# Performance work log

Measured on AMD Instinct MI355X. Metric: run time of the kernel, lower is better.

The kernel has to match this reference:

```python
import jax, jax.numpy as jnp
import numpy as np
import math

B, S, D, H, DFF = 4, 2048, 1024, 16, 4096
DK = D // 2  # 512; per-head dim = DK // H = 32
LN_EPS = 1e-3  # keras LayerNormalization default


def gelu_tanh(x):
    c = math.sqrt(2.0 / math.pi)
    return 0.5 * x * (1.0 + jnp.tanh(c * (x + 0.044715 * x * x * x)))


def layer_norm(z, g, b):
    mu = jnp.mean(z, axis=-1, keepdims=True)
    var = jnp.mean(jnp.square(z - mu), axis=-1, keepdims=True)
    return (z - mu) * jax.lax.rsqrt(var + LN_EPS) * g + b


def setup_inputs() -> dict:
    key = jax.random.key(0)
    ks = jax.random.split(key, 10)
    s = 0.02
    return {
        "x": jax.random.normal(ks[0], (B, S, D), dtype=jnp.float32),
        "mask": jnp.zeros((1, 1, S, S), dtype=jnp.float32),
        "Wq": jax.random.normal(ks[1], (D, DK), dtype=jnp.float32) * s,
        "bq": jnp.zeros((DK,), jnp.float32),
        "Wk": jax.random.normal(ks[2], (D, DK), dtype=jnp.float32) * s,
        "bk": jnp.zeros((DK,), jnp.float32),
        "Wv": jax.random.normal(ks[3], (D, DK), dtype=jnp.float32) * s,
        "bv": jnp.zeros((DK,), jnp.float32),
        "Wo": jax.random.normal(ks[4], (DK, D), dtype=jnp.float32) * s,
        "bo": jnp.zeros((D,), jnp.float32),
        "W1": jax.random.normal(ks[5], (D, DFF), dtype=jnp.float32) * s,
        "b1": jnp.zeros((DFF,), jnp.float32),
        "W2": jax.random.normal(ks[6], (DFF, D), dtype=jnp.float32) * s,
        "b2": jnp.zeros((D,), jnp.float32),
        "g1": jnp.ones((D,), jnp.float32),
        "be1": jnp.zeros((D,), jnp.float32),
        "g2": jnp.ones((D,), jnp.float32),
        "be2": jnp.zeros((D,), jnp.float32),
    }


def reference(x, mask, Wq, bq, Wk, bk, Wv, bv, Wo, bo, W1, b1, W2, b2, g1, be1, g2, be2):
    dh = DK // H
    # QKV projections: D -> DK total, split over H heads
    q = (x @ Wq + bq).reshape(B, S, H, dh).transpose(0, 2, 1, 3)  # [B,H,S,dh]
    k = (x @ Wk + bk).reshape(B, S, H, dh).transpose(0, 2, 1, 3)
    v = (x @ Wv + bv).reshape(B, S, H, dh).transpose(0, 2, 1, 3)
    # NOTE: source scales by sqrt(d_k)=sqrt(DK), not per-head dim
    scores = jnp.einsum("bhqd,bhkd->bhqk", q, k) / jnp.sqrt(jnp.asarray(DK, x.dtype))
    scores = scores + (-1e9) * mask
    w = jax.nn.softmax(scores, axis=-1)
    o = jnp.einsum("bhqk,bhkd->bhqd", w, v)  # [B,H,S,dh]
    o = o.transpose(0, 2, 1, 3).reshape(B, S, DK)
    attn_out = o @ Wo + bo  # [B,S,D]
    h1 = layer_norm(x + attn_out, g1, be1)
    # NOTE: source applies GELU AFTER the second Dense
    ff = gelu_tanh((h1 @ W1 + b1) @ W2 + b2)
    return layer_norm(h1 + ff, g2, be2)
```

## Files before the change

### kernel.cpp

```cpp
#include <hip/hip_runtime.h>

typedef unsigned short u16;
typedef unsigned int   u32;
typedef short s16x8 __attribute__((ext_vector_type(8)));
typedef float f32x4 __attribute__((ext_vector_type(4)));
typedef u32   u32x2 __attribute__((ext_vector_type(2)));
typedef s16x8 __attribute__((may_alias)) s16x8_a;
typedef f32x4 __attribute__((may_alias)) f32x4_a;
typedef u32x2 __attribute__((may_alias)) u32x2_a;

#define S_LEN   2048
#define D_MODEL 1024
#define DK_DIM  512
#define DFF_DIM 4096
#define MS_ROWS 8192

__device__ __forceinline__ u16 f2bf(float f) {
  union { float f; unsigned u; } x; x.f = f;
  unsigned r = x.u + 0x7fffu + ((x.u >> 16) & 1u);
  return (u16)(r >> 16);
}
__device__ __forceinline__ float bf2f(u16 u) {
  union { unsigned u; float f; } x; x.u = ((unsigned)u) << 16; return x.f;
}

__device__ __forceinline__ void gload_lds16(const void* g, void* l) {
  __builtin_amdgcn_global_load_lds(
      (const __attribute__((address_space(1))) unsigned int*)g,
      (__attribute__((address_space(3))) unsigned int*)l, 16, 0, 0);
}


__global__ __launch_bounds__(256)
void uber_prep(const float* __restrict__ x, u16* __restrict__ xb,
               const float* __restrict__ W1, u16* __restrict__ w1c,
               const float* __restrict__ Wq, const float* __restrict__ Wk,
               const float* __restrict__ Wv, u16* __restrict__ wqkvt,
               const float* __restrict__ Wo, u16* __restrict__ wot,
               const float* __restrict__ W2, u16* __restrict__ w2t)
{
  if (blockIdx.x < 2048) {
    const int na = MS_ROWS * D_MODEL;
    const int total = na + D_MODEL * DFF_DIM;
    const int stride = 2048 * 256 * 4;
    for (int i = (blockIdx.x * 256 + threadIdx.x) * 4; i < total; i += stride) {
      if (i < na) {
        float4 f = *(const float4*)&x[i];
        ushort4 u;
        u.x = f2bf(f.x); u.y = f2bf(f.y); u.z = f2bf(f.z); u.w = f2bf(f.w);
        *(ushort4*)&xb[i] = u;
      } else {
        float4 f = *(const float4*)&W1[i - na];
        ushort4 u;
        u.x = f2bf(f.x); u.y = f2bf(f.y); u.z = f2bf(f.z); u.w = f2bf(f.w);
        *(ushort4*)&w1c[i - na] = u;
      }
    }
    return;
  }
  __shared__ float T[64][65];
  const int t = blockIdx.x - 2048;
  const float* W; u16* Wt; int K, N, tile;
  if (t < 384) {
    int m = t >> 7; tile = t & 127;
    W = m == 0 ? Wq : (m == 1 ? Wk : Wv);
    Wt = wqkvt + (size_t)m * DK_DIM * D_MODEL;
    K = D_MODEL; N = DK_DIM;
  } else if (t < 512) {
    tile = t - 384; W = Wo; Wt = wot; K = DK_DIM; N = D_MODEL;
  } else {
    tile = t - 512; W = W2; Wt = w2t; K = DFF_DIM; N = D_MODEL;
  }
  const int ntiles_n = N >> 6;
  const int k0 = (tile / ntiles_n) * 64, n0 = (tile % ntiles_n) * 64;
  const int tr = threadIdx.x >> 4;
  const int tc = (threadIdx.x & 15) * 4;
#pragma unroll
  for (int i = 0; i < 4; i++) {
    float4 v = *(const float4*)&W[(size_t)(k0 + tr + i * 16) * N + n0 + tc];
    T[tr + i * 16][tc + 0] = v.x; T[tr + i * 16][tc + 1] = v.y;
    T[tr + i * 16][tc + 2] = v.z; T[tr + i * 16][tc + 3] = v.w;
  }
  __syncthreads();
#pragma unroll
  for (int i = 0; i < 4; i++) {
    int nrow = tr + i * 16;
    ushort4 u;
    u.x = f2bf(T[tc + 0][nrow]); u.y = f2bf(T[tc + 1][nrow]);
    u.z = f2bf(T[tc + 2][nrow]); u.w = f2bf(T[tc + 3][nrow]);
    *(ushort4*)&Wt[(size_t)(n0 + nrow) * K + k0 + tc] = u;
  }
}


template<int BM, int TBN, int OMODE, int GW>
__global__ __launch_bounds__(512, 2)
void gemm8(const u16* __restrict__ A, const u16* __restrict__ Bt,
           const float* __restrict__ b1p, const float* __restrict__ b2p,
           const float* __restrict__ b3p,
           float* __restrict__ Cf, u16* __restrict__ Cb,
           u16* __restrict__ Ck, u16* __restrict__ Cv,
           int M, int N, int K,
           const u16* __restrict__ rp, u16* __restrict__ rw,
           const float* __restrict__ rb1, const float* __restrict__ rb2,
           const u16* __restrict__ rw2t, float* __restrict__ rbc)
{
  if (GW > 0 && (int)blockIdx.x >= GW) {
    const int e = blockIdx.x - GW;
    const int rrow = e * 4 + (threadIdx.x >> 7);
    const int ei = (threadIdx.x & 127) * 8;
    const size_t base = (size_t)rrow * 1024 + ei;
    float sacc[8];
#pragma unroll
    for (int j = 0; j < 8; j++) sacc[j] = 0.f;
#pragma unroll
    for (int p = 0; p < 8; p++) {
      s16x8 v = *(const s16x8_a*)&rp[(size_t)p * 1048576 + base];
#pragma unroll
      for (int j = 0; j < 8; j++) sacc[j] += bf2f((u16)v[j]);
    }
    s16x8 ov;
#pragma unroll
    for (int j = 0; j < 8; j++) ov[j] = (short)f2bf(sacc[j]);
    *(s16x8_a*)&rw[base] = ov;
    const int wv = threadIdx.x >> 6;
    if (wv < 4) {
      const int n = e * 4 + wv;
      const int l = threadIdx.x & 63;
      float bs = 0.f;
      for (int d = l * 8; d < DFF_DIM; d += 64 * 8) {
        s16x8 v = *(const s16x8_a*)&rw2t[(size_t)n * DFF_DIM + d];
#pragma unroll
        for (int j = 0; j < 8; j++) bs += rb1[d + j] * bf2f((u16)v[j]);
      }
#pragma unroll
      for (int o = 32; o > 0; o >>= 1) bs += __shfl_down(bs, o, 64);
      if (l == 0) rbc[n] = bs + rb2[n];
    }
    return;
  }

  constexpr int NF = TBN / 64;
  constexpr int MF = BM / 32;
  constexpr int MFP = MF / 4;
  constexpr int LA = BM / 128;
  constexpr int LB = TBN / 128;
  constexpr int AHROWS = BM / 2;
  constexpr int BHROWS = TBN / 2;
  constexpr int AH_U = AHROWS * 64;
  constexpr int SLOT_B0 = BM * 64;
  constexpr int BUFU = BM * 64 + TBN * 64;
  __shared__ __align__(16) u16 lds[2 * BUFU];

  const int tid = threadIdx.x;
  const int l = tid & 63, w = tid >> 6;
  const int wrow = w >> 2, wcol = w & 3;
  const int fr = l & 15, g = l >> 4;

  const int nxt = N / TBN;
  const int nwg = (GW > 0) ? GW : gridDim.x;
  const int wg = (blockIdx.x & 7) * (nwg >> 3) + (blockIdx.x >> 3);
  const int n0 = (wg % nxt) * TBN;
  const int m0 = (wg / nxt) * BM;

  const int NT = K / 64;
  const int NITER = NT / 2;

  const int srow = l >> 3;
  const int sgc  = (l & 7) ^ srow;
  auto stageA = [&](int buf, int part, int kt) {
#pragma unroll
    for (int i = 0; i < LA; i++) {
      int row = i * 64 + w * 8 + srow;
      gload_lds16(A + (size_t)(m0 + part * AHROWS + row) * K + kt * 64 + sgc * 8,
                  (void*)&lds[buf * BUFU + part * AH_U + (i * 512 + w * 64) * 8]);
    }
  };
  auto stageB = [&](int buf, int part, int kt) {
#pragma unroll
    for (int i = 0; i < LB; i++) {
      int row = i * 64 + w * 8 + srow;
      gload_lds16(Bt + (size_t)(n0 + part * BHROWS + row) * K + kt * 64 + sgc * 8,
                  (void*)&lds[buf * BUFU + SLOT_B0 + part * (TBN * 32) + (i * 512 + w * 64) * 8]);
    }
  };

  f32x4 acc[MF][NF];
#pragma unroll
  for (int m = 0; m < MF; m++)
#pragma unroll
    for (int n = 0; n < NF; n++)
#pragma unroll
      for (int r = 0; r < 4; r++) acc[m][n][r] = 0.f;
  s16x8 bfrag[NF][2];

  stageA(0, 0, 0); stageA(0, 1, 0); stageB(0, 0, 0); stageB(0, 1, 0);
  stageB(1, 0, 1); stageB(1, 1, 1);
  if (LB == 2) asm volatile("s_waitcnt vmcnt(4)" ::: "memory");
  else         asm volatile("s_waitcnt vmcnt(2)" ::: "memory");
  __builtin_amdgcn_s_barrier();

  auto phase = [&](int buf, int q, auto stager, int vm) {
    s16x8 afr[MFP][2];
    const int abase = buf * BUFU + wrow * AH_U;
#pragma unroll
    for (int f2 = 0; f2 < MFP; f2++)
#pragma unroll
      for (int kk = 0; kk < 2; kk++)
        afr[f2][kk] = *(const s16x8_a*)
            &lds[abase + ((q * MFP + f2) * 16 + fr) * 64 + (((kk * 4 + g) ^ (fr & 7)) * 8)];
    if (q == 0) {
      const int bbase = buf * BUFU + SLOT_B0 + (wcol >> 1) * (TBN * 32) + (wcol & 1) * ((TBN / 4) * 64);
#pragma unroll
      for (int n = 0; n < NF; n++)
#pragma unroll
        for (int kk = 0; kk < 2; kk++)
          bfrag[n][kk] = *(const s16x8_a*)
              &lds[bbase + (n * 16 + fr) * 64 + (((kk * 4 + g) ^ (fr & 7)) * 8)];
    }
    stager();
    if (q == 0)
      asm volatile("s_waitcnt lgkmcnt(8)" ::: "memory");
    __builtin_amdgcn_s_barrier();
    asm volatile("s_waitcnt lgkmcnt(0)" ::: "memory");
    __builtin_amdgcn_sched_barrier(0);
    __builtin_amdgcn_s_setprio(1);
#pragma unroll
    for (int f2 = 0; f2 < MFP; f2++)
#pragma unroll
      for (int n = 0; n < NF; n++)
#pragma unroll
        for (int kk = 0; kk < 2; kk++)
          acc[q * MFP + f2][n] = __builtin_amdgcn_mfma_f32_16x16x32_bf16(
              afr[f2][kk], bfrag[n][kk], acc[q * MFP + f2][n], 0, 0, 0);
    __builtin_amdgcn_s_setprio(0);
    if (vm == 0)      asm volatile("s_waitcnt vmcnt(0)" ::: "memory");
    else if (vm == 2) asm volatile("s_waitcnt vmcnt(2)" ::: "memory");
    else if (vm == 4) asm volatile("s_waitcnt vmcnt(4)" ::: "memory");
    __builtin_amdgcn_s_barrier();
  };

  for (int j = 0; j < NITER; ++j) {
    const int t1 = 2 * j + 1;
    const bool more = (j + 1 < NITER);
    phase(0, 0, [&]{ stageA(1, 0, t1); }, -1);
    phase(0, 1, [&]{ stageA(1, 1, t1); }, -1);
    phase(0, 2, [&]{ if (more) stageB(0, 0, t1 + 1); }, -1);
    phase(0, 3, [&]{ if (more) stageB(0, 1, t1 + 1); }, more ? 2 * LB : 0);
    phase(1, 0, [&]{ if (more) stageA(0, 0, t1 + 1); }, -1);
    phase(1, 1, [&]{ if (more) stageA(0, 1, t1 + 1); }, -1);
    phase(1, 2, [&]{ if (more) stageB(1, 0, t1 + 2); }, -1);
    phase(1, 3, [&]{ if (more) stageB(1, 1, t1 + 2); }, more ? 2 * LB : -1);
  }

  const int rb = m0 + wrow * AHROWS + g * 4;
  const int cb = n0 + wcol * (TBN / 4) + fr;
#pragma unroll
  for (int m = 0; m < MF; m++) {
#pragma unroll
    for (int n = 0; n < NF; n++) {
      const int col = cb + n * 16;
      const int row0 = rb + m * 16;
      if (OMODE == 0) {
        float bz = b1p[col];
#pragma unroll
        for (int r = 0; r < 4; r++)
          Cb[(size_t)(row0 + r) * N + col] = f2bf(acc[m][n][r] + bz);
      } else if (OMODE == 1) {
        float bz = b1p[col];
#pragma unroll
        for (int r = 0; r < 4; r++)
          Cf[(size_t)(row0 + r) * N + col] = acc[m][n][r] + bz;
      } else {
        if (col < 512) {
          float bz = b1p[col];
#pragma unroll
          for (int r = 0; r < 4; r++)
            Cb[(size_t)(row0 + r) * 512 + col] =
                f2bf((acc[m][n][r] + bz) * (0.044194173824159216f * 1.4426950408889634f));
        } else if (col < 1024) {
          float bz = b2p[col - 512];
#pragma unroll
          for (int r = 0; r < 4; r++)
            Ck[(size_t)(row0 + r) * 512 + (col - 512)] = f2bf(acc[m][n][r] + bz);
        } else {
          float bz = b3p[col - 1024];
          const int cv = col - 1024;
          const int bb = row0 >> 11, ss = row0 & 2047;
          const int hd = cv >> 5, dd = cv & 31;
          ushort4 u4;
          u4.x = f2bf(acc[m][n][0] + bz);
          u4.y = f2bf(acc[m][n][1] + bz);
          u4.z = f2bf(acc[m][n][2] + bz);
          u4.w = f2bf(acc[m][n][3] + bz);
          *(ushort4*)&Cv[((size_t)(bb * 16 + hd) * 32 + dd) * 2048 + ss] = u4;
        }
      }
    }
  }
}


template<int OMODE, bool TRIBIAS>
__global__ __launch_bounds__(512, 4)
void gemmT(const u16* __restrict__ A, const u16* __restrict__ Bt,
           const float* __restrict__ b1p, const float* __restrict__ b2p,
           const float* __restrict__ b3p,
           float* __restrict__ Cf, u16* __restrict__ Cb,
           int M, int N, int Kblk, int lda, long partStride)
{
  __shared__ __align__(16) u16 lds[3 * 12288];

  const int tid = threadIdx.x;
  const int l = tid & 63, w = tid >> 6;
  const int wrow = w >> 2, wcol = w & 3;
  const int fr = l & 15, g = l >> 4;

  const int nxt = N >> 8;
  const int nwg = gridDim.x;
  const int wg = (blockIdx.x & 7) * (nwg >> 3) + (blockIdx.x >> 3);
  const int n0 = (wg % nxt) * 256;
  const int m0 = (wg / nxt) * 128;
  const long koff = (long)blockIdx.y * Kblk;

  const int NT = Kblk >> 5;

  const int srow = l >> 2;
  const int sck  = (l & 3) ^ ((l >> 3) & 3);
  auto stage = [&](int kt, int bi) {
    const long kb = koff + kt * 32 + sck * 8;
    gload_lds16(A + (size_t)(m0 + w * 16 + srow) * lda + kb,
                (void*)&lds[bi * 12288 + w * 512]);
    gload_lds16(Bt + (size_t)(n0 + w * 16 + srow) * lda + kb,
                (void*)&lds[bi * 12288 + 4096 + w * 512]);
    gload_lds16(Bt + (size_t)(n0 + 128 + w * 16 + srow) * lda + kb,
                (void*)&lds[bi * 12288 + 8192 + w * 512]);
  };

  f32x4 acc[4][4];
#pragma unroll
  for (int m = 0; m < 4; m++)
#pragma unroll
    for (int n = 0; n < 4; n++)
#pragma unroll
      for (int r = 0; r < 4; r++) acc[m][n][r] = 0.f;

  stage(0, 0);
  stage(1, 1);
  asm volatile("s_waitcnt vmcnt(3)" ::: "memory");
  __builtin_amdgcn_s_barrier();

  const int rsw = (g ^ ((fr >> 1) & 3)) * 8;
  int bi = 0;
  for (int t = 0; t < NT; ++t) {
    s16x8 afr[4], bfr[4];
    const int ab = bi * 12288 + fr * 32 + rsw;
#pragma unroll
    for (int m = 0; m < 4; m++)
      afr[m] = *(const s16x8_a*)&lds[ab + (wrow * 64 + m * 16) * 32];
#pragma unroll
    for (int n = 0; n < 4; n++)
      bfr[n] = *(const s16x8_a*)&lds[ab + 4096 + (wcol * 64 + n * 16) * 32];
    const bool more2 = (t + 2 < NT);
    if (more2) {
      int b2i = bi + 2; if (b2i >= 3) b2i -= 3;
      stage(t + 2, b2i);
    }
    asm volatile("s_waitcnt lgkmcnt(0)" ::: "memory");
    __builtin_amdgcn_sched_barrier(0);
    __builtin_amdgcn_s_setprio(1);
#pragma unroll
    for (int m = 0; m < 4; m++)
#pragma unroll
      for (int n = 0; n < 4; n++)
        acc[m][n] = __builtin_amdgcn_mfma_f32_16x16x32_bf16(afr[m], bfr[n], acc[m][n], 0, 0, 0);
    __builtin_amdgcn_s_setprio(0);
    if (more2)            asm volatile("s_waitcnt vmcnt(3)" ::: "memory");
    else if (t + 1 < NT)  asm volatile("s_waitcnt vmcnt(0)" ::: "memory");
    __builtin_amdgcn_s_barrier();
    bi = (bi + 1 == 3) ? 0 : bi + 1;
  }

  float* ldsf = (float*)lds;
  const bool dobias = (b1p != nullptr) && (blockIdx.y == 0);
#pragma unroll
  for (int p = 0; p < 2; p++) {
    if (p) __syncthreads();
    const int wb = w * 2180;
#pragma unroll
    for (int j = 0; j < 2; j++)
#pragma unroll
      for (int n = 0; n < 4; n++)
#pragma unroll
        for (int r = 0; r < 4; r++)
          ldsf[wb + (j * 16 + g * 4 + r) * 68 + n * 16 + fr] = acc[2 * p + j][n][r];
    __syncthreads();
#pragma unroll
    for (int i = 0; i < 8; i++) {
      int lin = i * 512 + tid;
      int rl = lin >> 6, ch = lin & 63;
      int row_g = m0 + 32 * p + (rl & 31) + (rl >> 5) * 64;
      int colbase = n0 + ch * 4;
      const float* src = &ldsf[((rl >> 5) * 4 + (ch >> 4)) * 2180 + (rl & 31) * 68 + (ch & 15) * 4];
      f32x4 v = *(const f32x4_a*)src;
      if (dobias) {
        const float* bp;
        int cb2;
        if (TRIBIAS) {
          bp = colbase < 512 ? b1p : (colbase < 1024 ? b2p : b3p);
          cb2 = colbase & 511;
        } else { bp = b1p; cb2 = colbase; }
        float4 bz = *(const float4*)&bp[cb2];
        v[0] += bz.x; v[1] += bz.y; v[2] += bz.z; v[3] += bz.w;
      }
      if (OMODE == 1) {
        *(float4*)&Cf[(size_t)row_g * N + colbase + blockIdx.y * partStride] =
            *(float4*)&v;
      } else if (OMODE == 3) {
        ushort4 u;
        u.x = f2bf(v[0]); u.y = f2bf(v[1]); u.z = f2bf(v[2]); u.w = f2bf(v[3]);
        *(ushort4*)&Cb[(size_t)row_g * N + colbase + blockIdx.y * partStride] = u;
      } else {
        ushort4 u;
        u.x = f2bf(v[0]); u.y = f2bf(v[1]); u.z = f2bf(v[2]); u.w = f2bf(v[3]);
        *(ushort4*)&Cb[(size_t)row_g * N + colbase] = u;
      }
    }
  }
}


__global__ __launch_bounds__(256, 4)
void flash_attn(const u16* __restrict__ q, const u16* __restrict__ k,
                const u16* __restrict__ vt, u16* __restrict__ o)
{
  __shared__ __align__(16) u16 Ks[2][64 * 32];
  __shared__ __align__(16) u16 Vts[2][32 * 72];
  __shared__ __align__(16) u32 Ps[4][2][16 * 36];
  const int tid = threadIdx.x;
  const int l = tid & 63, w = tid >> 6;
  const int fr = l & 15, g = l >> 4;
  const int fk = g * 8;
  const int bh = blockIdx.y;
  const int b = bh >> 4, head = bh & 15;
  const int s0 = blockIdx.x * 128;
  const size_t qk_base = (size_t)b * S_LEN * DK_DIM + (size_t)head * 32;
  const size_t vt_base = (size_t)bh * 32 * S_LEN;

  s16x8 qf[2];
#pragma unroll
  for (int hh = 0; hh < 2; hh++)
    qf[hh] = *(const s16x8_a*)&q[qk_base + (size_t)(s0 + w * 32 + hh * 16 + fr) * DK_DIM + fk];

  s16x8 ones;
#pragma unroll
  for (int j = 0; j < 8; j++) ones[j] = (short)0x3F80;

  f32x4 oacc[2][2];
  f32x4 osum[2];
#pragma unroll
  for (int hh = 0; hh < 2; hh++) {
#pragma unroll
    for (int nb = 0; nb < 2; nb++)
#pragma unroll
      for (int r = 0; r < 4; r++) oacc[hh][nb][r] = 0.f;
#pragma unroll
    for (int r = 0; r < 4; r++) osum[hh][r] = 0.f;
  }

  const int kc_row = w * 16 + (l >> 2);
  const int kc_col = ((l & 3) ^ ((l >> 3) & 3)) * 8;
  const int ksw = (g ^ ((fr >> 1) & 3)) * 8;
  const int vd = tid >> 3;
  const int vc = tid & 7;

  const int NTILE = S_LEN / 64;

  gload_lds16(&k[qk_base + (size_t)(0 + kc_row) * DK_DIM + kc_col], (void*)&Ks[0][w * 512]);
  {
    s16x8 vv0 = *(const s16x8_a*)&vt[vt_base + (size_t)vd * S_LEN + 0 + vc * 8];
    asm volatile("s_waitcnt vmcnt(0)" ::: "memory");
    *(s16x8_a*)&Vts[0][vd * 72 + vc * 8] = vv0;
  }
  __syncthreads();

  for (int t = 0; t < NTILE; t++) {
    const int cur = t & 1, nx = cur ^ 1;
    const bool more = (t + 1 < NTILE);
    s16x8 vv;
    if (more) {
      gload_lds16(&k[qk_base + (size_t)((t + 1) * 64 + kc_row) * DK_DIM + kc_col],
                  (void*)&Ks[nx][w * 512]);
      vv = *(const s16x8_a*)&vt[vt_base + (size_t)vd * S_LEN + (t + 1) * 64 + vc * 8];
    }

    s16x8 af[4], vf[2][2];
#pragma unroll
    for (int nb = 0; nb < 4; nb++)
      af[nb] = *(const s16x8_a*)&Ks[cur][(nb * 16 + fr) * 32 + ksw];
#pragma unroll
    for (int kk = 0; kk < 2; kk++)
#pragma unroll
      for (int nb = 0; nb < 2; nb++)
        vf[kk][nb] = *(const s16x8_a*)&Vts[cur][(nb * 16 + fr) * 72 + kk * 32 + fk];

    f32x4 sc[2][4];
    __builtin_amdgcn_s_setprio(1);
#pragma unroll
    for (int hh = 0; hh < 2; hh++)
#pragma unroll
      for (int nb = 0; nb < 4; nb++) {
        f32x4 z; z[0] = 0.f; z[1] = 0.f; z[2] = 0.f; z[3] = 0.f;
        sc[hh][nb] = __builtin_amdgcn_mfma_f32_16x16x32_bf16(af[nb], qf[hh], z, 0, 0, 0);
      }
    __builtin_amdgcn_s_setprio(0);
#pragma unroll
    for (int hh = 0; hh < 2; hh++)
#pragma unroll
      for (int nb = 0; nb < 4; nb++)
#pragma unroll
        for (int r = 0; r < 4; r++)
          sc[hh][nb][r] = __builtin_amdgcn_exp2f(sc[hh][nb][r]);
#pragma unroll
    for (int hh = 0; hh < 2; hh++)
#pragma unroll
      for (int nb = 0; nb < 4; nb++) {
        u32 pk0, pk1;
        asm("v_cvt_pk_bf16_f32 %0, %1, %2" : "=v"(pk0) : "v"(sc[hh][nb][0]), "v"(sc[hh][nb][1]));
        asm("v_cvt_pk_bf16_f32 %0, %1, %2" : "=v"(pk1) : "v"(sc[hh][nb][2]), "v"(sc[hh][nb][3]));
        u32x2 pr; pr.x = pk0; pr.y = pk1;
        *(u32x2_a*)&Ps[w][hh][fr * 36 + nb * 8 + g * 2] = pr;
      }
    __builtin_amdgcn_s_setprio(1);
#pragma unroll
    for (int hh = 0; hh < 2; hh++)
#pragma unroll
      for (int kk = 0; kk < 2; kk++) {
        s16x8 pf = *(const s16x8_a*)&Ps[w][hh][fr * 36 + kk * 16 + g * 4];
#pragma unroll
        for (int nb = 0; nb < 2; nb++)
          oacc[hh][nb] = __builtin_amdgcn_mfma_f32_16x16x32_bf16(pf, vf[kk][nb], oacc[hh][nb], 0, 0, 0);
        osum[hh] = __builtin_amdgcn_mfma_f32_16x16x32_bf16(pf, ones, osum[hh], 0, 0, 0);
      }
    __builtin_amdgcn_s_setprio(0);

    if (more) {
      asm volatile("s_waitcnt vmcnt(0)" ::: "memory");
      *(s16x8_a*)&Vts[nx][vd * 72 + vc * 8] = vv;
    }
    __syncthreads();
  }

#pragma unroll
  for (int hh = 0; hh < 2; hh++)
#pragma unroll
    for (int nb = 0; nb < 2; nb++)
#pragma unroll
      for (int r = 0; r < 4; r++) {
        int row = s0 + w * 32 + hh * 16 + g * 4 + r;
        o[qk_base + (size_t)row * DK_DIM + nb * 16 + fr] = f2bf(oacc[hh][nb][r] / osum[hh][r]);
      }
}


__global__ __launch_bounds__(256)
void ln_res(const u16* __restrict__ xb, const u16* __restrict__ attnb,
            const float* __restrict__ g, const float* __restrict__ be,
            u16* __restrict__ h1b)
{
  __shared__ float red[8];
  const int row = blockIdx.x;
  const int c4 = threadIdx.x * 4;
  const size_t bidx = (size_t)row * D_MODEL + c4;
  ushort4 xa = *(const ushort4*)&xb[bidx];
  ushort4 ab = *(const ushort4*)&attnb[bidx];
  float z0 = bf2f(xa.x) + bf2f(ab.x);
  float z1 = bf2f(xa.y) + bf2f(ab.y);
  float z2 = bf2f(xa.z) + bf2f(ab.z);
  float z3 = bf2f(xa.w) + bf2f(ab.w);
  float s = z0 + z1 + z2 + z3;
  float s2 = z0 * z0 + z1 * z1 + z2 * z2 + z3 * z3;
#pragma unroll
  for (int o = 32; o > 0; o >>= 1) { s += __shfl_down(s, o, 64); s2 += __shfl_down(s2, o, 64); }
  const int w = threadIdx.x >> 6;
  if ((threadIdx.x & 63) == 0) { red[w] = s; red[4 + w] = s2; }
  __syncthreads();
  s  = red[0] + red[1] + red[2] + red[3];
  s2 = red[4] + red[5] + red[6] + red[7];
  float mu = s * (1.f / D_MODEL);
  float var = s2 * (1.f / D_MODEL) - mu * mu;
  float rs = rsqrtf(var + 1e-3f);
  float4 gv = *(const float4*)&g[c4];
  float4 bv = *(const float4*)&be[c4];
  ushort4 hb;
  hb.x = f2bf((z0 - mu) * rs * gv.x + bv.x);
  hb.y = f2bf((z1 - mu) * rs * gv.y + bv.y);
  hb.z = f2bf((z2 - mu) * rs * gv.z + bv.z);
  hb.w = f2bf((z3 - mu) * rs * gv.w + bv.w);
  *(ushort4*)&h1b[bidx] = hb;
}

__device__ __forceinline__ float gelu_t(float u) {
  float t = tanhf(0.7978845608028654f * (u + 0.044715f * u * u * u));
  return 0.5f * u * (1.f + t);
}

__global__ __launch_bounds__(256)
void ln_gelu(float* __restrict__ out, const u16* __restrict__ ffcb,
             const u16* __restrict__ h1b,
             const float* __restrict__ g, const float* __restrict__ be)
{
  __shared__ float red[8];
  const int row = blockIdx.x;
  const int c4 = threadIdx.x * 4;
  const size_t bidx = (size_t)row * D_MODEL + c4;
  ushort4 fa = *(const ushort4*)&ffcb[bidx];
  ushort4 hb = *(const ushort4*)&h1b[bidx];
  float z0 = bf2f(hb.x) + gelu_t(bf2f(fa.x));
  float z1 = bf2f(hb.y) + gelu_t(bf2f(fa.y));
  float z2 = bf2f(hb.z) + gelu_t(bf2f(fa.z));
  float z3 = bf2f(hb.w) + gelu_t(bf2f(fa.w));
  float s = z0 + z1 + z2 + z3;
  float s2 = z0 * z0 + z1 * z1 + z2 * z2 + z3 * z3;
#pragma unroll
  for (int o = 32; o > 0; o >>= 1) { s += __shfl_down(s, o, 64); s2 += __shfl_down(s2, o, 64); }
  const int w = threadIdx.x >> 6;
  if ((threadIdx.x & 63) == 0) { red[w] = s; red[4 + w] = s2; }
  __syncthreads();
  s  = red[0] + red[1] + red[2] + red[3];
  s2 = red[4] + red[5] + red[6] + red[7];
  float mu = s * (1.f / D_MODEL);
  float var = s2 * (1.f / D_MODEL) - mu * mu;
  float rs = rsqrtf(var + 1e-3f);
  float4 gv = *(const float4*)&g[c4];
  float4 bv = *(const float4*)&be[c4];
  float4 ov;
  ov.x = (z0 - mu) * rs * gv.x + bv.x;
  ov.y = (z1 - mu) * rs * gv.y + bv.y;
  ov.z = (z2 - mu) * rs * gv.z + bv.z;
  ov.w = (z3 - mu) * rs * gv.w + bv.w;
  *(float4*)&out[bidx] = ov;
}


extern "C" void kernel_launch(void* const* d_in, const int* in_sizes, int n_in,
                              void* d_out, int out_size, void* d_ws, size_t ws_size,
                              hipStream_t stream)
{
  const float* x   = (const float*)d_in[0];
  const float* Wq  = (const float*)d_in[2];
  const float* bq  = (const float*)d_in[3];
  const float* Wk  = (const float*)d_in[4];
  const float* bk  = (const float*)d_in[5];
  const float* Wv  = (const float*)d_in[6];
  const float* bv  = (const float*)d_in[7];
  const float* Wo  = (const float*)d_in[8];
  const float* bo  = (const float*)d_in[9];
  const float* W1  = (const float*)d_in[10];
  const float* b1  = (const float*)d_in[11];
  const float* W2  = (const float*)d_in[12];
  const float* b2  = (const float*)d_in[13];
  const float* g1  = (const float*)d_in[14];
  const float* be1 = (const float*)d_in[15];
  const float* g2  = (const float*)d_in[16];
  const float* be2 = (const float*)d_in[17];
  float* out = (float*)d_out;

  char* ws = (char*)d_ws;
  size_t off = 0;
  auto alloc = [&](size_t bytes) -> void* {
    void* p = ws + off;
    off += (bytes + 255) & ~(size_t)255;
    return p;
  };
  u16*   xb    = (u16*)  alloc((size_t)MS_ROWS * D_MODEL * 2);
  u16*   qb    = (u16*)  alloc((size_t)MS_ROWS * DK_DIM * 2);
  u16*   kbuf  = (u16*)  alloc((size_t)MS_ROWS * DK_DIM * 2);
  u16*   vtb   = (u16*)  alloc((size_t)64 * 32 * S_LEN * 2);
  u16*   obuf  = (u16*)  alloc((size_t)MS_ROWS * DK_DIM * 2);
  u16*   wqkvt = (u16*)  alloc((size_t)3 * DK_DIM * D_MODEL * 2);
  u16*   wot   = (u16*)  alloc((size_t)DK_DIM * D_MODEL * 2);
  u16*   w1c   = (u16*)  alloc((size_t)D_MODEL * DFF_DIM * 2);
  u16*   w2t   = (u16*)  alloc((size_t)DFF_DIM * D_MODEL * 2);
  u16*   wct   = (u16*)  alloc((size_t)D_MODEL * D_MODEL * 2);
  u16*   attnb = (u16*)  alloc((size_t)MS_ROWS * D_MODEL * 2);
  u16*   ffcb  = (u16*)  alloc((size_t)MS_ROWS * D_MODEL * 2);
  u16*   h1b   = (u16*)  alloc((size_t)MS_ROWS * D_MODEL * 2);
  float* bc    = (float*)alloc(1024 * 4);
  u16*   wctp  = attnb;

  uber_prep<<<2048 + 1536, 256, 0, stream>>>(
      x, xb, W1, w1c, Wq, Wk, Wv, wqkvt, Wo, wot, W2, w2t);

  gemmT<3, false><<<dim3((1024 / 128) * (1024 / 256), 8), 512, 0, stream>>>(
      w2t, w1c, nullptr, nullptr, nullptr, nullptr, wctp,
      1024, 1024, DFF_DIM / 8, DFF_DIM, (long)(1024 * 1024));

  gemm8<128, 256, 2, 384><<<384 + 256, 512, 0, stream>>>(
      xb, wqkvt, bq, bk, bv, nullptr, qb, kbuf, vtb, MS_ROWS, 1536, D_MODEL,
      wctp, wct, b1, b2, w2t, bc);

  flash_attn<<<dim3(S_LEN / 128, 64), 256, 0, stream>>>(qb, kbuf, vtb, obuf);

  gemm8<128, 256, 0, 0><<<(MS_ROWS / 128) * (D_MODEL / 256), 512, 0, stream>>>(
      obuf, wot, bo, bo, bo, nullptr, attnb, nullptr, nullptr, MS_ROWS, D_MODEL, DK_DIM,
      nullptr, nullptr, nullptr, nullptr, nullptr, nullptr);

  ln_res<<<MS_ROWS, 256, 0, stream>>>(xb, attnb, g1, be1, h1b);

  gemm8<128, 256, 0, 0><<<(MS_ROWS / 128) * (D_MODEL / 256), 512, 0, stream>>>(
      h1b, wct, bc, bc, bc, nullptr, ffcb, nullptr, nullptr, MS_ROWS, D_MODEL, D_MODEL,
      nullptr, nullptr, nullptr, nullptr, nullptr, nullptr);

  ln_gelu<<<MS_ROWS, 256, 0, stream>>>(out, ffcb, h1b, g2, be2);
}
```

Measured before the change: 198.9 us.

## Rewrite flash attention with 32x32x16 MFMA and register-resident P via lane shuffles

Moves the attention kernel from 16x16x32 bf16 MFMAs to 32x32x16 MFMAs, where each wave computes a 32x64 score tile in two accumulators. The softmax probabilities are no longer staged through LDS. They are packed to bf16 and rearranged across half-waves with shfl_xor so they can feed the PV MFMA directly. K now uses a padded LDS layout filled by register loads instead of direct global-to-LDS loads, and the occupancy hint drops from 4 to 3 blocks per CU to cover the larger accumulators. This trades the LDS round-trip and bank conflicts for extra cross-lane shuffles, higher register pressure and lower occupancy.

```diff
diff --git a/kernel.cpp b/kernel.cpp
--- a/kernel.cpp
+++ b/kernel.cpp
@@ -3,9 +3,13 @@
 typedef unsigned short u16;
 typedef unsigned int   u32;
 typedef short s16x8 __attribute__((ext_vector_type(8)));
+typedef short s16x4 __attribute__((ext_vector_type(4)));
 typedef float f32x4 __attribute__((ext_vector_type(4)));
+typedef float f32x16 __attribute__((ext_vector_type(16)));
 typedef u32   u32x2 __attribute__((ext_vector_type(2)));
+typedef u32   u32x4 __attribute__((ext_vector_type(4)));
 typedef s16x8 __attribute__((may_alias)) s16x8_a;
+typedef s16x4 __attribute__((may_alias)) s16x4_a;
 typedef f32x4 __attribute__((may_alias)) f32x4_a;
 typedef u32x2 __attribute__((may_alias)) u32x2_a;
 
@@ -430,17 +434,15 @@
 }
 
 
-__global__ __launch_bounds__(256, 4)
+__global__ __launch_bounds__(256, 3)
 void flash_attn(const u16* __restrict__ q, const u16* __restrict__ k,
                 const u16* __restrict__ vt, u16* __restrict__ o)
 {
-  __shared__ __align__(16) u16 Ks[2][64 * 32];
-  __shared__ __align__(16) u16 Vts[2][32 * 72];
-  __shared__ __align__(16) u32 Ps[4][2][16 * 36];
+  __shared__ __align__(16) u16 KL[2][64 * 36];
+  __shared__ __align__(16) u16 VL[2][32 * 72];
   const int tid = threadIdx.x;
   const int l = tid & 63, w = tid >> 6;
-  const int fr = l & 15, g = l >> 4;
-  const int fk = g * 8;
+  const int col = l & 31, hi = l >> 5;
   const int bh = blockIdx.y;
   const int b = bh >> 4, head = bh & 15;
   const int s0 = blockIdx.x * 128;
@@ -448,118 +450,119 @@
   const size_t vt_base = (size_t)bh * 32 * S_LEN;
 
   s16x8 qf[2];
-#pragma unroll
-  for (int hh = 0; hh < 2; hh++)
-    qf[hh] = *(const s16x8_a*)&q[qk_base + (size_t)(s0 + w * 32 + hh * 16 + fr) * DK_DIM + fk];
+  {
+    const int qrow = s0 + w * 32 + col;
+#pragma unroll
+    for (int s = 0; s < 2; s++)
+      qf[s] = *(const s16x8_a*)&q[qk_base + (size_t)qrow * DK_DIM + s * 16 + hi * 8];
+  }
 
   s16x8 ones;
 #pragma unroll
   for (int j = 0; j < 8; j++) ones[j] = (short)0x3F80;
 
-  f32x4 oacc[2][2];
-  f32x4 osum[2];
-#pragma unroll
-  for (int hh = 0; hh < 2; hh++) {
-#pragma unroll
-    for (int nb = 0; nb < 2; nb++)
-#pragma unroll
-      for (int r = 0; r < 4; r++) oacc[hh][nb][r] = 0.f;
-#pragma unroll
-    for (int r = 0; r < 4; r++) osum[hh][r] = 0.f;
-  }
-
-  const int kc_row = w * 16 + (l >> 2);
-  const int kc_col = ((l & 3) ^ ((l >> 3) & 3)) * 8;
-  const int ksw = (g ^ ((fr >> 1) & 3)) * 8;
-  const int vd = tid >> 3;
-  const int vc = tid & 7;
+  f32x16 oacc, osum;
+#pragma unroll
+  for (int r = 0; r < 16; r++) { oacc[r] = 0.f; osum[r] = 0.f; }
+
+  const int krow = tid >> 2, kc8 = (tid & 3) * 8;
+  const int vd = tid >> 3,  vkv = (tid & 7) * 8;
+  const u16* kp = k + qk_base + (size_t)krow * DK_DIM + kc8;
+  const u16* vp = vt + vt_base + (size_t)vd * S_LEN + vkv;
+
+  {
+    s16x8 kr = *(const s16x8_a*)kp; kp += (size_t)64 * DK_DIM;
+    s16x8 vr = *(const s16x8_a*)vp; vp += 64;
+    s16x4 klo, khi;
+#pragma unroll
+    for (int j = 0; j < 4; j++) { klo[j] = kr[j]; khi[j] = kr[4 + j]; }
+    *(s16x4_a*)&KL[0][krow * 36 + kc8]     = klo;
+    *(s16x4_a*)&KL[0][krow * 36 + kc8 + 4] = khi;
+    *(s16x8_a*)&VL[0][vd * 72 + vkv] = vr;
+  }
+  __syncthreads();
 
   const int NTILE = S_LEN / 64;
-
-  gload_lds16(&k[qk_base + (size_t)(0 + kc_row) * DK_DIM + kc_col], (void*)&Ks[0][w * 512]);
-  {
-    s16x8 vv0 = *(const s16x8_a*)&vt[vt_base + (size_t)vd * S_LEN + 0 + vc * 8];
-    asm volatile("s_waitcnt vmcnt(0)" ::: "memory");
-    *(s16x8_a*)&Vts[0][vd * 72 + vc * 8] = vv0;
-  }
-  __syncthreads();
-
   for (int t = 0; t < NTILE; t++) {
     const int cur = t & 1, nx = cur ^ 1;
     const bool more = (t + 1 < NTILE);
-    s16x8 vv;
+    s16x8 krn, vrn;
     if (more) {
-      gload_lds16(&k[qk_base + (size_t)((t + 1) * 64 + kc_row) * DK_DIM + kc_col],
-                  (void*)&Ks[nx][w * 512]);
-      vv = *(const s16x8_a*)&vt[vt_base + (size_t)vd * S_LEN + (t + 1) * 64 + vc * 8];
-    }
-
-    s16x8 af[4], vf[2][2];
-#pragma unroll
-    for (int nb = 0; nb < 4; nb++)
-      af[nb] = *(const s16x8_a*)&Ks[cur][(nb * 16 + fr) * 32 + ksw];
-#pragma unroll
-    for (int kk = 0; kk < 2; kk++)
-#pragma unroll
-      for (int nb = 0; nb < 2; nb++)
-        vf[kk][nb] = *(const s16x8_a*)&Vts[cur][(nb * 16 + fr) * 72 + kk * 32 + fk];
-
-    f32x4 sc[2][4];
+      krn = *(const s16x8_a*)kp; kp += (size_t)64 * DK_DIM;
+      vrn = *(const s16x8_a*)vp; vp += 64;
+    }
+
+    s16x8 ka[2][2];
+#pragma unroll
+    for (int c = 0; c < 2; c++)
+#pragma unroll
+      for (int s = 0; s < 2; s++) {
+        const int base = (c * 32 + col) * 36 + s * 16 + hi * 8;
+        s16x4 lo = *(const s16x4_a*)&KL[cur][base];
+        s16x4 hi4 = *(const s16x4_a*)&KL[cur][base + 4];
+#pragma unroll
+        for (int j = 0; j < 4; j++) { ka[c][s][j] = lo[j]; ka[c][s][4 + j] = hi4[j]; }
+      }
+    s16x8 vb[4];
+#pragma unroll
+    for (int ks = 0; ks < 4; ks++)
+      vb[ks] = *(const s16x8_a*)&VL[cur][col * 72 + ks * 16 + hi * 8];
+
+    f32x16 sc0, sc1;
+#pragma unroll
+    for (int r = 0; r < 16; r++) { sc0[r] = 0.f; sc1[r] = 0.f; }
     __builtin_amdgcn_s_setprio(1);
-#pragma unroll
-    for (int hh = 0; hh < 2; hh++)
-#pragma unroll
-      for (int nb = 0; nb < 4; nb++) {
-        f32x4 z; z[0] = 0.f; z[1] = 0.f; z[2] = 0.f; z[3] = 0.f;
-        sc[hh][nb] = __builtin_amdgcn_mfma_f32_16x16x32_bf16(af[nb], qf[hh], z, 0, 0, 0);
-      }
+    sc0 = __builtin_amdgcn_mfma_f32_32x32x16_bf16(ka[0][0], qf[0], sc0, 0, 0, 0);
+    sc0 = __builtin_amdgcn_mfma_f32_32x32x16_bf16(ka[0][1], qf[1], sc0, 0, 0, 0);
+    sc1 = __builtin_amdgcn_mfma_f32_32x32x16_bf16(ka[1][0], qf[0], sc1, 0, 0, 0);
+    sc1 = __builtin_amdgcn_mfma_f32_32x32x16_bf16(ka[1][1], qf[1], sc1, 0, 0, 0);
     __builtin_amdgcn_s_setprio(0);
 #pragma unroll
-    for (int hh = 0; hh < 2; hh++)
-#pragma unroll
-      for (int nb = 0; nb < 4; nb++)
-#pragma unroll
-        for (int r = 0; r < 4; r++)
-          sc[hh][nb][r] = __builtin_amdgcn_exp2f(sc[hh][nb][r]);
-#pragma unroll
-    for (int hh = 0; hh < 2; hh++)
-#pragma unroll
-      for (int nb = 0; nb < 4; nb++) {
-        u32 pk0, pk1;
-        asm("v_cvt_pk_bf16_f32 %0, %1, %2" : "=v"(pk0) : "v"(sc[hh][nb][0]), "v"(sc[hh][nb][1]));
-        asm("v_cvt_pk_bf16_f32 %0, %1, %2" : "=v"(pk1) : "v"(sc[hh][nb][2]), "v"(sc[hh][nb][3]));
-        u32x2 pr; pr.x = pk0; pr.y = pk1;
-        *(u32x2_a*)&Ps[w][hh][fr * 36 + nb * 8 + g * 2] = pr;
-      }
-    __builtin_amdgcn_s_setprio(1);
-#pragma unroll
-    for (int hh = 0; hh < 2; hh++)
-#pragma unroll
-      for (int kk = 0; kk < 2; kk++) {
-        s16x8 pf = *(const s16x8_a*)&Ps[w][hh][fr * 36 + kk * 16 + g * 4];
-#pragma unroll
-        for (int nb = 0; nb < 2; nb++)
-          oacc[hh][nb] = __builtin_amdgcn_mfma_f32_16x16x32_bf16(pf, vf[kk][nb], oacc[hh][nb], 0, 0, 0);
-        osum[hh] = __builtin_amdgcn_mfma_f32_16x16x32_bf16(pf, ones, osum[hh], 0, 0, 0);
-      }
-    __builtin_amdgcn_s_setprio(0);
+    for (int r = 0; r < 16; r++) {
+      sc0[r] = __builtin_amdgcn_exp2f(sc0[r]);
+      sc1[r] = __builtin_amdgcn_exp2f(sc1[r]);
+    }
+    u32 cp[2][8];
+#pragma unroll
+    for (int i = 0; i < 8; i++) {
+      asm("v_cvt_pk_bf16_f32 %0, %1, %2" : "=v"(cp[0][i]) : "v"(sc0[2 * i]), "v"(sc0[2 * i + 1]));
+      asm("v_cvt_pk_bf16_f32 %0, %1, %2" : "=v"(cp[1][i]) : "v"(sc1[2 * i]), "v"(sc1[2 * i + 1]));
+    }
+#pragma unroll
+    for (int ks = 0; ks < 4; ks++) {
+      const int c = ks >> 1, h = (ks & 1) * 4;
+      u32 a0 = cp[c][h], a1 = cp[c][h + 1], a2 = cp[c][h + 2], a3 = cp[c][h + 3];
+      u32 x0 = (u32)__shfl_xor((int)a0, 32, 64);
+      u32 x1 = (u32)__shfl_xor((int)a1, 32, 64);
+      u32 x2 = (u32)__shfl_xor((int)a2, 32, 64);
+      u32 x3 = (u32)__shfl_xor((int)a3, 32, 64);
+      u32x4 pw;
+      pw.x = hi ? x2 : a0;
+      pw.y = hi ? x3 : a1;
+      pw.z = hi ? a2 : x0;
+      pw.w = hi ? a3 : x1;
+      s16x8 pa = __builtin_bit_cast(s16x8, pw);
+      oacc = __builtin_amdgcn_mfma_f32_32x32x16_bf16(pa, vb[ks], oacc, 0, 0, 0);
+      osum = __builtin_amdgcn_mfma_f32_32x32x16_bf16(pa, ones, osum, 0, 0, 0);
+    }
 
     if (more) {
-      asm volatile("s_waitcnt vmcnt(0)" ::: "memory");
-      *(s16x8_a*)&Vts[nx][vd * 72 + vc * 8] = vv;
+      s16x4 klo, khi;
+#pragma unroll
+      for (int j = 0; j < 4; j++) { klo[j] = krn[j]; khi[j] = krn[4 + j]; }
+      *(s16x4_a*)&KL[nx][krow * 36 + kc8]     = klo;
+      *(s16x4_a*)&KL[nx][krow * 36 + kc8 + 4] = khi;
+      *(s16x8_a*)&VL[nx][vd * 72 + vkv] = vrn;
     }
     __syncthreads();
   }
 
 #pragma unroll
-  for (int hh = 0; hh < 2; hh++)
-#pragma unroll
-    for (int nb = 0; nb < 2; nb++)
-#pragma unroll
-      for (int r = 0; r < 4; r++) {
-        int row = s0 + w * 32 + hh * 16 + g * 4 + r;
-        o[qk_base + (size_t)row * DK_DIM + nb * 16 + fr] = f2bf(oacc[hh][nb][r] / osum[hh][r]);
-      }
+  for (int r = 0; r < 16; r++) {
+    int qrow = (r & 3) + 8 * (r >> 2) + 4 * hi;
+    int row = s0 + w * 32 + qrow;
+    o[qk_base + (size_t)row * DK_DIM + col] = f2bf(oacc[r] / osum[r]);
+  }
 }
 
 
```

Measured after the change: 202.8 us. About the same (+1.9%).
